# Performance work log

Hardware: AMD Instinct MI355X
Metric: run time of the kernel (lower is better)

The kernel has to match this reference:

```python
import jax, jax.numpy as jnp
import numpy as np


def setup_inputs() -> dict:
    key = jax.random.key(0)
    kx, ky, kw = jax.random.split(key, 3)
    B, N, M = 8, 4096, 4096
    x = jax.random.normal(kx, (B, N, 3), dtype=jnp.float32)
    y = jax.random.normal(ky, (B, M, 3), dtype=jnp.float32)
    weight = jax.random.uniform(kw, (B,), dtype=jnp.float32)
    return {"x": x, "y": y, "weight": weight}


def reference(x, y, weight):
    # (mathematically identical to sum((x-y)^2), avoids the (B,N,M,3) tensor)
    x2 = jnp.sum(x * x, axis=-1)                     # (B, N)
    y2 = jnp.sum(y * y, axis=-1)                     # (B, M)
    xy = jnp.einsum('bnd,bmd->bnm', x, y)            # (B, N, M)
    dist = jnp.maximum(x2[:, :, None] + y2[:, None, :] - 2.0 * xy, 0.0)
    dist_x_min = jnp.min(dist, axis=2)               # (B, N) nearest-in-y per x
    dist_y_min = jnp.min(dist, axis=1)               # (B, M) nearest-in-x per y
    # point_reduction='mean', bidirectional=True
    loss = jnp.mean(dist_x_min, axis=1) + jnp.mean(dist_y_min, axis=1)  # (B,)
    loss = loss * weight
    # batch_reduction='mean'
    return jnp.mean(loss)
```

## Files before the change

### kernel.cpp

```cpp
#include <hip/hip_runtime.h>
#include <math.h>


constexpr int BATCH = 8;
constexpr int NP    = 4096;
constexpr int MC    = 8;
constexpr int MCH   = 512;
constexpr int XC    = 4;
constexpr int KPT   = 4;
constexpr int T     = 256;

constexpr size_t PMIN_STRIDE = (size_t)BATCH * MC * NP;
constexpr size_t PS_OFF      = 2 * PMIN_STRIDE;

__global__ __launch_bounds__(T) void chamfer_partial(
    const float* __restrict__ x, const float* __restrict__ y,
    float* __restrict__ ws)
{
    const int bid = blockIdx.x;
    const int dir = bid >> 8;
    const int r   = bid & 255;
    const int b   = r >> 5;
    const int xc  = (r >> 3) & 3;
    const int mc  = r & 7;

    const float* q = dir ? y : x;
    const float* t = dir ? x : y;

    __shared__ float4 ty[MCH];
    const int tid = threadIdx.x;

    const float* tb = t + (size_t)(b * NP + mc * MCH) * 3;
    for (int j = tid; j < MCH; j += T) {
        float y0 = tb[3 * j + 0];
        float y1 = tb[3 * j + 1];
        float y2 = tb[3 * j + 2];
        ty[j] = make_float4(y0, y1, y2, fmaf(y0, y0, fmaf(y1, y1, y2 * y2)));
    }

    const int n0 = b * NP + xc * 1024 + tid * KPT;
    const float4* qb = reinterpret_cast<const float4*>(q + (size_t)n0 * 3);
    float4 qa = qb[0], q1 = qb[1], q2 = qb[2];
    float px[KPT][3] = {
        {qa.x, qa.y, qa.z},
        {qa.w, q1.x, q1.y},
        {q1.z, q1.w, q2.x},
        {q2.y, q2.z, q2.w},
    };
    float xn[KPT][3], x2s[KPT];
    #pragma unroll
    for (int k = 0; k < KPT; ++k) {
        x2s[k] = fmaf(px[k][0], px[k][0], fmaf(px[k][1], px[k][1], px[k][2] * px[k][2]));
        #pragma unroll
        for (int d = 0; d < 3; ++d) xn[k][d] = -2.0f * px[k][d];
    }

    __syncthreads();

    float mn[KPT] = {INFINITY, INFINITY, INFINITY, INFINITY};
    #pragma unroll 8
    for (int j = 0; j < MCH; ++j) {
        float4 tv = ty[j];
        #pragma unroll
        for (int k = 0; k < KPT; ++k) {
            float d = x2s[k] + tv.w;
            d = fmaf(xn[k][0], tv.x, d);
            d = fmaf(xn[k][1], tv.y, d);
            d = fmaf(xn[k][2], tv.z, d);
            mn[k] = fminf(mn[k], d);
        }
    }

    float4 out;
    out.x = fmaxf(mn[0], 0.0f);
    out.y = fmaxf(mn[1], 0.0f);
    out.z = fmaxf(mn[2], 0.0f);
    out.w = fmaxf(mn[3], 0.0f);

    float* pm = ws + (size_t)dir * PMIN_STRIDE
                   + ((size_t)(b * MC + mc)) * NP
                   + (size_t)xc * 1024 + (size_t)tid * KPT;
    *reinterpret_cast<float4*>(pm) = out;
}

__global__ __launch_bounds__(T) void chamfer_combine(
    const float* __restrict__ ws, float* __restrict__ ps)
{
    const int bid = blockIdx.x;
    const int dir = bid >> 5;
    const int b   = (bid >> 2) & 7;
    const int nq  = bid & 3;
    const int tid = threadIdx.x;

    const float* base = ws + (size_t)dir * PMIN_STRIDE + (size_t)b * MC * NP;

    float sum = 0.0f;
    #pragma unroll
    for (int i = 0; i < 4; ++i) {
        const int n = nq * 1024 + i * 256 + tid;
        float v = INFINITY;
        #pragma unroll
        for (int m = 0; m < MC; ++m) v = fminf(v, base[(size_t)m * NP + n]);
        sum += v;
    }

    for (int off = 32; off; off >>= 1) sum += __shfl_down(sum, off, 64);
    __shared__ float red[4];
    if ((tid & 63) == 0) red[tid >> 6] = sum;
    __syncthreads();
    if (tid == 0) ps[bid] = (red[0] + red[1]) + (red[2] + red[3]);
}

__global__ void chamfer_final(
    const float* __restrict__ ps, const float* __restrict__ w,
    float* __restrict__ out)
{
    const int l = threadIdx.x;
    float v = ps[l];
    const int b = (l >> 2) & 7;
    float acc = v * w[b] * (1.0f / ((float)NP * (float)BATCH));
    for (int off = 32; off; off >>= 1) acc += __shfl_down(acc, off, 64);
    if (l == 0) out[0] = acc;
}

extern "C" void kernel_launch(void* const* d_in, const int* in_sizes, int n_in,
                              void* d_out, int out_size, void* d_ws, size_t ws_size,
                              hipStream_t stream) {
    const float* x = (const float*)d_in[0];
    const float* y = (const float*)d_in[1];
    const float* w = (const float*)d_in[2];
    float* out = (float*)d_out;
    float* ws  = (float*)d_ws;

    chamfer_partial<<<2 * BATCH * XC * MC, T, 0, stream>>>(x, y, ws);
    chamfer_combine<<<64, T, 0, stream>>>(ws, ws + PS_OFF);
    chamfer_final<<<1, 64, 0, stream>>>(ws + PS_OFF, w, out);
}
```

Before: 32.40 us.

## Raise per-thread query count to 8 and hoist x-norm out of inner loop

Result: faster. 30.42 us (-6.1%).

```diff
diff --git a/kernel.cpp b/kernel.cpp
--- a/kernel.cpp
+++ b/kernel.cpp
@@ -4,10 +4,9 @@
 
 constexpr int BATCH = 8;
 constexpr int NP    = 4096;
-constexpr int MC    = 8;
-constexpr int MCH   = 512;
-constexpr int XC    = 4;
-constexpr int KPT   = 4;
+constexpr int MC    = 16;
+constexpr int MCH   = 256;
+constexpr int KPT   = 8;
 constexpr int T     = 256;
 
 constexpr size_t PMIN_STRIDE = (size_t)BATCH * MC * NP;
@@ -21,8 +20,8 @@
     const int dir = bid >> 8;
     const int r   = bid & 255;
     const int b   = r >> 5;
-    const int xc  = (r >> 3) & 3;
-    const int mc  = r & 7;
+    const int xc  = (r >> 4) & 1;
+    const int mc  = r & 15;
 
     const float* q = dir ? y : x;
     const float* t = dir ? x : y;
@@ -31,56 +30,60 @@
     const int tid = threadIdx.x;
 
     const float* tb = t + (size_t)(b * NP + mc * MCH) * 3;
-    for (int j = tid; j < MCH; j += T) {
-        float y0 = tb[3 * j + 0];
-        float y1 = tb[3 * j + 1];
-        float y2 = tb[3 * j + 2];
-        ty[j] = make_float4(y0, y1, y2, fmaf(y0, y0, fmaf(y1, y1, y2 * y2)));
+    {
+        float t0 = tb[3 * tid + 0];
+        float t1 = tb[3 * tid + 1];
+        float t2 = tb[3 * tid + 2];
+        ty[tid] = make_float4(t0, t1, t2, fmaf(t0, t0, fmaf(t1, t1, t2 * t2)));
     }
 
-    const int n0 = b * NP + xc * 1024 + tid * KPT;
+    const int n0 = b * NP + xc * 2048 + tid * KPT;
     const float4* qb = reinterpret_cast<const float4*>(q + (size_t)n0 * 3);
-    float4 qa = qb[0], q1 = qb[1], q2 = qb[2];
+    float4 v0 = qb[0], v1 = qb[1], v2 = qb[2], v3 = qb[3], v4 = qb[4], v5 = qb[5];
     float px[KPT][3] = {
-        {qa.x, qa.y, qa.z},
-        {qa.w, q1.x, q1.y},
-        {q1.z, q1.w, q2.x},
-        {q2.y, q2.z, q2.w},
+        {v0.x, v0.y, v0.z}, {v0.w, v1.x, v1.y},
+        {v1.z, v1.w, v2.x}, {v2.y, v2.z, v2.w},
+        {v3.x, v3.y, v3.z}, {v3.w, v4.x, v4.y},
+        {v4.z, v4.w, v5.x}, {v5.y, v5.z, v5.w},
     };
-    float xn[KPT][3], x2s[KPT];
+    float xn[KPT][3], x2s[KPT], mn[KPT];
     #pragma unroll
     for (int k = 0; k < KPT; ++k) {
         x2s[k] = fmaf(px[k][0], px[k][0], fmaf(px[k][1], px[k][1], px[k][2] * px[k][2]));
         #pragma unroll
         for (int d = 0; d < 3; ++d) xn[k][d] = -2.0f * px[k][d];
+        mn[k] = INFINITY;
     }
 
     __syncthreads();
 
-    float mn[KPT] = {INFINITY, INFINITY, INFINITY, INFINITY};
-    #pragma unroll 8
+    #pragma unroll 4
     for (int j = 0; j < MCH; ++j) {
         float4 tv = ty[j];
         #pragma unroll
         for (int k = 0; k < KPT; ++k) {
-            float d = x2s[k] + tv.w;
+            float d = fmaf(xn[k][2], tv.z, tv.w);
+            d = fmaf(xn[k][1], tv.y, d);
             d = fmaf(xn[k][0], tv.x, d);
-            d = fmaf(xn[k][1], tv.y, d);
-            d = fmaf(xn[k][2], tv.z, d);
             mn[k] = fminf(mn[k], d);
         }
     }
 
-    float4 out;
-    out.x = fmaxf(mn[0], 0.0f);
-    out.y = fmaxf(mn[1], 0.0f);
-    out.z = fmaxf(mn[2], 0.0f);
-    out.w = fmaxf(mn[3], 0.0f);
+    float4 o0, o1;
+    o0.x = fmaxf(x2s[0] + mn[0], 0.0f);
+    o0.y = fmaxf(x2s[1] + mn[1], 0.0f);
+    o0.z = fmaxf(x2s[2] + mn[2], 0.0f);
+    o0.w = fmaxf(x2s[3] + mn[3], 0.0f);
+    o1.x = fmaxf(x2s[4] + mn[4], 0.0f);
+    o1.y = fmaxf(x2s[5] + mn[5], 0.0f);
+    o1.z = fmaxf(x2s[6] + mn[6], 0.0f);
+    o1.w = fmaxf(x2s[7] + mn[7], 0.0f);
 
     float* pm = ws + (size_t)dir * PMIN_STRIDE
                    + ((size_t)(b * MC + mc)) * NP
-                   + (size_t)xc * 1024 + (size_t)tid * KPT;
-    *reinterpret_cast<float4*>(pm) = out;
+                   + (size_t)xc * 2048 + (size_t)tid * KPT;
+    reinterpret_cast<float4*>(pm)[0] = o0;
+    reinterpret_cast<float4*>(pm)[1] = o1;
 }
 
 __global__ __launch_bounds__(T) void chamfer_combine(
@@ -132,7 +135,7 @@
     float* out = (float*)d_out;
     float* ws  = (float*)d_ws;
 
-    chamfer_partial<<<2 * BATCH * XC * MC, T, 0, stream>>>(x, y, ws);
+    chamfer_partial<<<512, T, 0, stream>>>(x, y, ws);
     chamfer_combine<<<64, T, 0, stream>>>(ws, ws + PS_OFF);
     chamfer_final<<<1, 64, 0, stream>>>(ws + PS_OFF, w, out);
 }
```

## Fuse partial min and combine by staging full target cloud in LDS

Applied to the files above, without the earlier changes.

After: 90.46 us. +179.2%, slower.

```diff
diff --git a/kernel.cpp b/kernel.cpp
--- a/kernel.cpp
+++ b/kernel.cpp
@@ -4,123 +4,86 @@
 
 constexpr int BATCH = 8;
 constexpr int NP    = 4096;
-constexpr int MC    = 8;
-constexpr int MCH   = 512;
-constexpr int XC    = 4;
-constexpr int KPT   = 4;
-constexpr int T     = 256;
+constexpr int T     = 512;
+constexpr int QPB   = 256;
+constexpr int HALF  = 2048;
 
-constexpr size_t PMIN_STRIDE = (size_t)BATCH * MC * NP;
-constexpr size_t PS_OFF      = 2 * PMIN_STRIDE;
-
-__global__ __launch_bounds__(T) void chamfer_partial(
+__global__ __launch_bounds__(T) void chamfer_main(
     const float* __restrict__ x, const float* __restrict__ y,
-    float* __restrict__ ws)
+    const float* __restrict__ w, float* __restrict__ ps)
 {
     const int bid = blockIdx.x;
-    const int dir = bid >> 8;
-    const int r   = bid & 255;
-    const int b   = r >> 5;
-    const int xc  = (r >> 3) & 3;
-    const int mc  = r & 7;
+    const int dir = bid >> 7;
+    const int b   = (bid >> 4) & 7;
+    const int qc  = bid & 15;
 
     const float* q = dir ? y : x;
     const float* t = dir ? x : y;
 
-    __shared__ float4 ty[MCH];
+    __shared__ float4 ty[NP];
+    __shared__ float  red[QPB];
+    __shared__ float  rsum[8];
+
     const int tid = threadIdx.x;
 
-    const float* tb = t + (size_t)(b * NP + mc * MCH) * 3;
-    for (int j = tid; j < MCH; j += T) {
-        float y0 = tb[3 * j + 0];
-        float y1 = tb[3 * j + 1];
-        float y2 = tb[3 * j + 2];
-        ty[j] = make_float4(y0, y1, y2, fmaf(y0, y0, fmaf(y1, y1, y2 * y2)));
+    const float* tb = t + (size_t)b * NP * 3;
+    for (int j = tid; j < NP; j += T) {
+        float t0 = tb[3 * j + 0];
+        float t1 = tb[3 * j + 1];
+        float t2 = tb[3 * j + 2];
+        ty[j] = make_float4(t0, t1, t2, fmaf(t0, t0, fmaf(t1, t1, t2 * t2)));
     }
 
-    const int n0 = b * NP + xc * 1024 + tid * KPT;
-    const float4* qb = reinterpret_cast<const float4*>(q + (size_t)n0 * 3);
-    float4 qa = qb[0], q1 = qb[1], q2 = qb[2];
-    float px[KPT][3] = {
-        {qa.x, qa.y, qa.z},
-        {qa.w, q1.x, q1.y},
-        {q1.z, q1.w, q2.x},
-        {q2.y, q2.z, q2.w},
-    };
-    float xn[KPT][3], x2s[KPT];
-    #pragma unroll
-    for (int k = 0; k < KPT; ++k) {
-        x2s[k] = fmaf(px[k][0], px[k][0], fmaf(px[k][1], px[k][1], px[k][2] * px[k][2]));
-        #pragma unroll
-        for (int d = 0; d < 3; ++d) xn[k][d] = -2.0f * px[k][d];
-    }
+    const int ql   = tid & (QPB - 1);
+    const int half = tid >> 8;
+    const int n0   = b * NP + qc * QPB + ql;
+    const float q0 = q[3 * n0 + 0];
+    const float q1 = q[3 * n0 + 1];
+    const float q2 = q[3 * n0 + 2];
+    const float x2  = fmaf(q0, q0, fmaf(q1, q1, q2 * q2));
+    const float xn0 = -2.0f * q0, xn1 = -2.0f * q1, xn2 = -2.0f * q2;
 
     __syncthreads();
 
-    float mn[KPT] = {INFINITY, INFINITY, INFINITY, INFINITY};
-    #pragma unroll 8
-    for (int j = 0; j < MCH; ++j) {
-        float4 tv = ty[j];
-        #pragma unroll
-        for (int k = 0; k < KPT; ++k) {
-            float d = x2s[k] + tv.w;
-            d = fmaf(xn[k][0], tv.x, d);
-            d = fmaf(xn[k][1], tv.y, d);
-            d = fmaf(xn[k][2], tv.z, d);
-            mn[k] = fminf(mn[k], d);
-        }
+    float mn = INFINITY;
+    const int j0 = half * HALF;
+    #pragma unroll 4
+    for (int j = j0; j < j0 + HALF; j += 2) {
+        float4 ta = ty[j];
+        float4 tc = ty[j + 1];
+        float da = fmaf(xn0, ta.x, fmaf(xn1, ta.y, fmaf(xn2, ta.z, ta.w)));
+        float db = fmaf(xn0, tc.x, fmaf(xn1, tc.y, fmaf(xn2, tc.z, tc.w)));
+        mn = fminf(mn, fminf(da, db));
     }
 
-    float4 out;
-    out.x = fmaxf(mn[0], 0.0f);
-    out.y = fmaxf(mn[1], 0.0f);
-    out.z = fmaxf(mn[2], 0.0f);
-    out.w = fmaxf(mn[3], 0.0f);
+    if (half == 1) red[ql] = mn;
+    __syncthreads();
+    float val = 0.0f;
+    if (half == 0) {
+        float m = fminf(mn, red[ql]);
+        val = fmaxf(x2 + m, 0.0f);
+    }
 
-    float* pm = ws + (size_t)dir * PMIN_STRIDE
-                   + ((size_t)(b * MC + mc)) * NP
-                   + (size_t)xc * 1024 + (size_t)tid * KPT;
-    *reinterpret_cast<float4*>(pm) = out;
+    for (int off = 32; off; off >>= 1) val += __shfl_down(val, off, 64);
+    if ((tid & 63) == 0) rsum[tid >> 6] = val;
+    __syncthreads();
+    if (tid == 0) {
+        float s = ((rsum[0] + rsum[1]) + (rsum[2] + rsum[3]))
+                + ((rsum[4] + rsum[5]) + (rsum[6] + rsum[7]));
+        ps[bid] = s * w[b] * (1.0f / ((float)NP * (float)BATCH));
+    }
 }
 
-__global__ __launch_bounds__(T) void chamfer_combine(
-    const float* __restrict__ ws, float* __restrict__ ps)
+__global__ __launch_bounds__(256) void chamfer_final(
+    const float* __restrict__ ps, float* __restrict__ out)
 {
-    const int bid = blockIdx.x;
-    const int dir = bid >> 5;
-    const int b   = (bid >> 2) & 7;
-    const int nq  = bid & 3;
     const int tid = threadIdx.x;
-
-    const float* base = ws + (size_t)dir * PMIN_STRIDE + (size_t)b * MC * NP;
-
-    float sum = 0.0f;
-    #pragma unroll
-    for (int i = 0; i < 4; ++i) {
-        const int n = nq * 1024 + i * 256 + tid;
-        float v = INFINITY;
-        #pragma unroll
-        for (int m = 0; m < MC; ++m) v = fminf(v, base[(size_t)m * NP + n]);
-        sum += v;
-    }
-
-    for (int off = 32; off; off >>= 1) sum += __shfl_down(sum, off, 64);
+    float v = ps[tid];
+    for (int off = 32; off; off >>= 1) v += __shfl_down(v, off, 64);
     __shared__ float red[4];
-    if ((tid & 63) == 0) red[tid >> 6] = sum;
+    if ((tid & 63) == 0) red[tid >> 6] = v;
     __syncthreads();
-    if (tid == 0) ps[bid] = (red[0] + red[1]) + (red[2] + red[3]);
-}
-
-__global__ void chamfer_final(
-    const float* __restrict__ ps, const float* __restrict__ w,
-    float* __restrict__ out)
-{
-    const int l = threadIdx.x;
-    float v = ps[l];
-    const int b = (l >> 2) & 7;
-    float acc = v * w[b] * (1.0f / ((float)NP * (float)BATCH));
-    for (int off = 32; off; off >>= 1) acc += __shfl_down(acc, off, 64);
-    if (l == 0) out[0] = acc;
+    if (tid == 0) out[0] = (red[0] + red[1]) + (red[2] + red[3]);
 }
 
 extern "C" void kernel_launch(void* const* d_in, const int* in_sizes, int n_in,
@@ -130,9 +93,8 @@
     const float* y = (const float*)d_in[1];
     const float* w = (const float*)d_in[2];
     float* out = (float*)d_out;
-    float* ws  = (float*)d_ws;
+    float* ps  = (float*)d_ws;
 
-    chamfer_partial<<<2 * BATCH * XC * MC, T, 0, stream>>>(x, y, ws);
-    chamfer_combine<<<64, T, 0, stream>>>(ws, ws + PS_OFF);
-    chamfer_final<<<1, 64, 0, stream>>>(ws + PS_OFF, w, out);
+    chamfer_main<<<256, T, 0, stream>>>(x, y, w, ps);
+    chamfer_final<<<1, 256, 0, stream>>>(ps, out);
 }
```
